# Kernel tuning notes

Measured on AMD Instinct MI355X. Metric: run time of the kernel, lower is better.

The kernel has to match this reference:

```python
import jax, jax.numpy as jnp
import numpy as np

EMBED_DIMS = [8, 16, 8]      # prod = 1024 = embed_dim
HIDDEN_DIMS = [16, 16, 16]   # prod = 4096 = hidden_dim
RANK = 16
B, S = 4, 1024


def _make_cores(key, in_dims, out_dims, rank):
    d = len(in_dims)
    ranks = [1] + [rank] * (d - 1) + [1]
    cores = []
    for k in range(d):
        key, sub = jax.random.split(key)
        shape = (ranks[k], in_dims[k], out_dims[k], ranks[k + 1])
        scale = 1.0 / np.sqrt(in_dims[k] * ranks[k])
        cores.append((scale * jax.random.normal(sub, shape, dtype=jnp.float32)))
    return cores


def setup_inputs() -> dict:
    key = jax.random.key(0)
    k_x, k1, k2, kb1, kb2 = jax.random.split(key, 5)
    x = jax.random.normal(k_x, (B, S, 1024), dtype=jnp.float32)
    fc1 = _make_cores(k1, EMBED_DIMS, HIDDEN_DIMS, RANK)
    fc2 = _make_cores(k2, HIDDEN_DIMS, EMBED_DIMS, RANK)
    b1 = 0.01 * jax.random.normal(kb1, (4096,), dtype=jnp.float32)
    b2 = 0.01 * jax.random.normal(kb2, (1024,), dtype=jnp.float32)
    return {
        "x": x,
        "fc1_c0": fc1[0], "fc1_c1": fc1[1], "fc1_c2": fc1[2], "fc1_b": b1,
        "fc2_c0": fc2[0], "fc2_c1": fc2[1], "fc2_c2": fc2[2], "fc2_b": b2,
    }


def tt_linear(x_flat, cores, bias, in_dims):
    """TT-matrix x batch-of-vectors product. x_flat: [N, prod(in_dims)].

    Cores: core_k has shape [r_{k-1}, n_k, m_k, r_k] with r_0 = r_d = 1.
    Invariant: acc is [r_{k-1}, n_k, rest] with rest laid out as
    (n_{k+1}..n_d, N, m_1..m_{k-1}).
    """
    N = x_flat.shape[0]
    acc = x_flat.reshape((N,) + tuple(in_dims))      # [N, n1..nd]
    acc = jnp.moveaxis(acc, 0, -1)                   # [n1..nd, N]
    acc = acc.reshape(in_dims[0], -1)[None]          # [1, n1, rest]
    d = len(cores)
    for k, c in enumerate(cores):
        # contract previous rank + current input mode
        acc = jnp.einsum('pnR,pnmq->Rmq', acc, c)    # [rest, m_k, r_k]
        if k < d - 1:
            n_next = in_dims[k + 1]
            R, m, q = acc.shape
            acc = acc.reshape(n_next, R // n_next, m, q)
            acc = jnp.transpose(acc, (3, 0, 1, 2)).reshape(q, n_next, -1)
    # final acc: [N * m1..m_{d-1}, m_d, 1] -> [N, M]
    return acc.reshape(N, -1) + bias


def reference(x, fc1_c0, fc1_c1, fc1_c2, fc1_b, fc2_c0, fc2_c1, fc2_c2, fc2_b):
    flat = x.reshape(-1, x.shape[-1])                        # [N, embed_dim]
    z1 = tt_linear(flat, [fc1_c0, fc1_c1, fc1_c2], fc1_b, EMBED_DIMS)   # [N, hidden]
    h1 = jax.nn.gelu(z1, approximate=False)                  # exact erf GELU (torch default)
    z2 = tt_linear(h1, [fc2_c0, fc2_c1, fc2_c2], fc2_b, HIDDEN_DIMS)    # [N, embed]
    return z2.reshape(*x.shape[:-1], z2.shape[-1])
```

## Files before the change

### kernel.cpp

```cpp
#include <hip/hip_runtime.h>
#include <stdint.h>

__device__ __forceinline__ float b2f(unsigned short u) {
    union { uint32_t i; float f; } v; v.i = ((uint32_t)u) << 16; return v.f;
}
__device__ __forceinline__ unsigned short f2b(float f) {
    union { float f; uint32_t i; } v; v.f = f;
    uint32_t r = v.i + 0x7fffu + ((v.i >> 16) & 1u);
    return (unsigned short)(r >> 16);
}

typedef __bf16 bf16x8 __attribute__((ext_vector_type(8)));
typedef float  f32x16 __attribute__((ext_vector_type(16)));

template<int N3, int M3>
__device__ __forceinline__ void build_T_body(int e,
                                             const float* __restrict__ c1,
                                             const float* __restrict__ c2,
                                             float* __restrict__ T) {
    int m3 = e % M3;
    int t  = e / M3;
    int n3 = t % N3;
    int rm = t / N3;
    float s = 0.f;
#pragma unroll
    for (int r2 = 0; r2 < 16; ++r2)
        s += c1[rm * 16 + r2] * c2[(r2 * N3 + n3) * M3 + m3];
    T[e] = s;
}

__global__ __launch_bounds__(256)
void prep_stage1(const float* __restrict__ c11, const float* __restrict__ c12,
                 float* __restrict__ T1,
                 const float* __restrict__ c21, const float* __restrict__ c22,
                 float* __restrict__ T2,
                 const float* __restrict__ x, unsigned short* __restrict__ xb) {
    const int b = blockIdx.x;
    if (b < 2048) {
        build_T_body<8, 16>(b * 256 + threadIdx.x, c11, c12, T1);
    } else if (b < 4096) {
        build_T_body<16, 8>((b - 2048) * 256 + threadIdx.x, c21, c22, T2);
    } else {
        const int t = (b - 4096) * 256 + threadIdx.x;
        const float4* p = (const float4*)(x + (size_t)t * 8);
        float4 f0 = p[0], f1 = p[1];
        int4 o;
        o.x = (uint32_t)f2b(f0.x) | ((uint32_t)f2b(f0.y) << 16);
        o.y = (uint32_t)f2b(f0.z) | ((uint32_t)f2b(f0.w) << 16);
        o.z = (uint32_t)f2b(f1.x) | ((uint32_t)f2b(f1.y) << 16);
        o.w = (uint32_t)f2b(f1.z) | ((uint32_t)f2b(f1.w) << 16);
        ((int4*)xb)[t] = o;
    }
}

template<int N1, int N2, int N3, int M1, int M2, int M3>
__device__ __forceinline__ void build_W_body(int t,
                                             const float* __restrict__ c0,
                                             const float* __restrict__ T,
                                             unsigned short* __restrict__ W) {
    constexpr int K = N1 * N2 * N3;
    int m3 = t % M3;
    int m2 = (t / M3) % M2;
    int n2 = (t / (M3 * M2)) % N2;
    int m1 = (t / (M3 * M2 * N2)) % M1;
    int n1 =  t / (M3 * M2 * N2 * M1);

    float c0r[16];
    const float4* c0p = (const float4*)(c0 + (n1 * M1 + m1) * 16);
#pragma unroll
    for (int i = 0; i < 4; ++i) ((float4*)c0r)[i] = c0p[i];

    float acc[N3] = {};
#pragma unroll
    for (int r1 = 0; r1 < 16; ++r1) {
        const float* Tp = T + (size_t)(((r1 * 16 + n2) * 16 + m2) * N3) * M3 + m3;
#pragma unroll
        for (int n3 = 0; n3 < N3; ++n3)
            acc[n3] += c0r[r1] * Tp[n3 * M3];
    }

    unsigned short ob[N3];
#pragma unroll
    for (int n3 = 0; n3 < N3; ++n3) ob[n3] = f2b(acc[n3]);

    unsigned short* dst = W + (size_t)((m1 * M2 + m2) * M3 + m3) * K
                            + (n1 * N2 + n2) * N3;
#pragma unroll
    for (int c = 0; c < N3 / 8; ++c)
        ((int4*)dst)[c] = ((const int4*)ob)[c];
}

__global__ __launch_bounds__(256)
void build_W_both(const float* __restrict__ c10, const float* __restrict__ T1,
                  unsigned short* __restrict__ W1,
                  const float* __restrict__ c20, const float* __restrict__ T2,
                  unsigned short* __restrict__ W2) {
    const int b = blockIdx.x;
    if (b < 2048)
        build_W_body<8, 16, 8, 16, 16, 16>(b * 256 + threadIdx.x, c10, T1, W1);
    else
        build_W_body<16, 16, 16, 8, 16, 8>((b - 2048) * 256 + threadIdx.x, c20, T2, W2);
}

template<int N1, int N2, int N3, int M1, int M2, int M3>
__global__ __launch_bounds__(256)
void build_W(const float* __restrict__ c0, const float* __restrict__ T,
             unsigned short* __restrict__ W) {
    build_W_body<N1, N2, N3, M1, M2, M3>(blockIdx.x * 256 + threadIdx.x, c0, T, W);
}

#define PC_COMPUTE(BUF)                                                       \
    {                                                                         \
        _Pragma("unroll")                                                     \
        for (int ks = 0; ks < 4; ++ks) {                                      \
            bf16x8 a_f[FI], b_f[FJ];                                          \
            _Pragma("unroll")                                                 \
            for (int i = 0; i < FI; ++i) {                                    \
                const int key = (m32 & 7) ^                                   \
                    (((waveM >> 3) + 4 * i + (m32 >> 3)) & 7);                \
                const int slot = ((ks * 2 + khalf) ^ key) * 8;                \
                a_f[i] = *(const bf16x8*)&As[(BUF) * ASZ +                    \
                          (waveM + i * 32 + m32) * BK + slot];                \
            }                                                                 \
            _Pragma("unroll")                                                 \
            for (int j = 0; j < FJ; ++j) {                                    \
                const int key = (m32 & 7) ^                                   \
                    (((waveN >> 3) + 4 * j + (m32 >> 3)) & 7);                \
                const int slot = ((ks * 2 + khalf) ^ key) * 8;                \
                b_f[j] = *(const bf16x8*)&Bs[(BUF) * BSZ +                    \
                          (waveN + j * 32 + m32) * BK + slot];                \
            }                                                                 \
            _Pragma("unroll")                                                 \
            for (int i = 0; i < FI; ++i)                                      \
                _Pragma("unroll")                                             \
                for (int j = 0; j < FJ; ++j)                                  \
                    acc[i][j] = __builtin_amdgcn_mfma_f32_32x32x16_bf16(      \
                        a_f[i], b_f[j], acc[i][j], 0, 0, 0);                  \
        }                                                                     \
    }

template<int BM, int BN, int KTOT, bool DO_GELU, bool A_F32, bool C_F32>
__global__ __launch_bounds__(512, 4)
void gemm_pc(const void* __restrict__ Av,
             const unsigned short* __restrict__ Bt,
             const float* __restrict__ bias,
             void* __restrict__ Cv,
             int Ncols) {
    constexpr int BK  = 64;
    constexpr int CA  = BM / 8;
    constexpr int CB  = BN / 8;
    constexpr int PA  = CA / 4;
    constexpr int PB  = CB / 4;
    constexpr int FI  = BM / 64;
    constexpr int FJ  = BN / 64;
    constexpr int ASZ = BM * BK;
    constexpr int BSZ = BN * BK;
    __shared__ unsigned short As[2 * ASZ];
    __shared__ unsigned short Bs[2 * BSZ];

    const int tid  = threadIdx.x;
    const int lane = tid & 63;
    const int wave = tid >> 6;
    const int rowBase = blockIdx.y * BM;
    const int colBase = blockIdx.x * BN;

    const int lr    = lane >> 3;
    const int jj    = lane & 7;
    const int m32   = lane & 31;
    const int khalf = lane >> 5;

    if (wave >= 4) {
        const int pw = wave - 4;

#pragma unroll
        for (int it = 0; it < PA; ++it) {
            const int c  = pw * PA + it;
            const int jg = jj ^ lr ^ (c & 7);
            const size_t aoff = (size_t)(rowBase + c * 8 + lr) * KTOT + jg * 8;
            int4 v;
            if (A_F32) {
                const float* ga = (const float*)Av + aoff;
                float4 f0 = *(const float4*)ga;
                float4 f1 = *(const float4*)(ga + 4);
                v.x = (uint32_t)f2b(f0.x) | ((uint32_t)f2b(f0.y) << 16);
                v.y = (uint32_t)f2b(f0.z) | ((uint32_t)f2b(f0.w) << 16);
                v.z = (uint32_t)f2b(f1.x) | ((uint32_t)f2b(f1.y) << 16);
                v.w = (uint32_t)f2b(f1.z) | ((uint32_t)f2b(f1.w) << 16);
            } else {
                v = *(const int4*)((const unsigned short*)Av + aoff);
            }
            *(int4*)&As[c * 512 + lane * 8] = v;
        }
#pragma unroll
        for (int it = 0; it < PB; ++it) {
            const int c  = pw * PB + it;
            const int jg = jj ^ lr ^ (c & 7);
            *(int4*)&Bs[c * 512 + lane * 8] =
                *(const int4*)(Bt + (size_t)(colBase + c * 8 + lr) * KTOT + jg * 8);
        }
        __syncthreads();

        int buf = 1;
        for (int k0 = BK; k0 < KTOT; k0 += BK) {
            int4 aR[PA], bR[PB];
#pragma unroll
            for (int it = 0; it < PA; ++it) {
                const int c  = pw * PA + it;
                const int jg = jj ^ lr ^ (c & 7);
                const size_t aoff = (size_t)(rowBase + c * 8 + lr) * KTOT + k0 + jg * 8;
                if (A_F32) {
                    const float* ga = (const float*)Av + aoff;
                    float4 f0 = *(const float4*)ga;
                    float4 f1 = *(const float4*)(ga + 4);
                    int4 v;
                    v.x = (uint32_t)f2b(f0.x) | ((uint32_t)f2b(f0.y) << 16);
                    v.y = (uint32_t)f2b(f0.z) | ((uint32_t)f2b(f0.w) << 16);
                    v.z = (uint32_t)f2b(f1.x) | ((uint32_t)f2b(f1.y) << 16);
                    v.w = (uint32_t)f2b(f1.z) | ((uint32_t)f2b(f1.w) << 16);
                    aR[it] = v;
                } else {
                    aR[it] = *(const int4*)((const unsigned short*)Av + aoff);
                }
            }
#pragma unroll
            for (int it = 0; it < PB; ++it) {
                const int c  = pw * PB + it;
                const int jg = jj ^ lr ^ (c & 7);
                bR[it] = *(const int4*)(Bt + (size_t)(colBase + c * 8 + lr) * KTOT + k0 + jg * 8);
            }
#pragma unroll
            for (int it = 0; it < PA; ++it) {
                const int c = pw * PA + it;
                *(int4*)&As[buf * ASZ + c * 512 + lane * 8] = aR[it];
            }
#pragma unroll
            for (int it = 0; it < PB; ++it) {
                const int c = pw * PB + it;
                *(int4*)&Bs[buf * BSZ + c * 512 + lane * 8] = bR[it];
            }
            __syncthreads();
            buf ^= 1;
        }
    } else {
        const int waveM = (wave >> 1) * (BM / 2);
        const int waveN = (wave & 1) * (BN / 2);
        f32x16 acc[FI][FJ] = {};

        __syncthreads();

        int cur = 0;
        for (int k0 = BK; k0 < KTOT; k0 += BK) {
            PC_COMPUTE(cur)
            __syncthreads();
            cur ^= 1;
        }
        PC_COMPUTE(cur)

#pragma unroll
        for (int i = 0; i < FI; ++i) {
#pragma unroll
            for (int j = 0; j < FJ; ++j) {
                const int col = colBase + waveN + j * 32 + m32;
                const float bv = bias[col];
#pragma unroll
                for (int reg = 0; reg < 16; ++reg) {
                    const int row = rowBase + waveM + i * 32 +
                                    (reg & 3) + 8 * (reg >> 2) + 4 * khalf;
                    float z = acc[i][j][reg] + bv;
                    if (DO_GELU)
                        z = 0.5f * z * (1.f + erff(z * 0.70710678118654752f));
                    const size_t off = (size_t)row * Ncols + col;
                    if (C_F32) ((float*)Cv)[off] = z;
                    else       ((unsigned short*)Cv)[off] = f2b(z);
                }
            }
        }
    }
}

extern "C" void kernel_launch(void* const* d_in, const int* in_sizes, int n_in,
                              void* d_out, int out_size, void* d_ws, size_t ws_size,
                              hipStream_t stream) {
    const float* x      = (const float*)d_in[0];
    const float* fc1_c0 = (const float*)d_in[1];
    const float* fc1_c1 = (const float*)d_in[2];
    const float* fc1_c2 = (const float*)d_in[3];
    const float* fc1_b  = (const float*)d_in[4];
    const float* fc2_c0 = (const float*)d_in[5];
    const float* fc2_c1 = (const float*)d_in[6];
    const float* fc2_c2 = (const float*)d_in[7];
    const float* fc2_b  = (const float*)d_in[8];

    float* T1 = (float*)d_out;
    float* T2 = (float*)d_out + 524288;
    unsigned short* xb = (unsigned short*)((char*)d_out + (4u << 20));

    char* ws = (char*)d_ws;
    const bool big = ws_size >= (48ull << 20);

    prep_stage1<<<6144, 256, 0, stream>>>(fc1_c1, fc1_c2, T1,
                                          fc2_c1, fc2_c2, T2, x, xb);

    if (big) {
        unsigned short* W1 = (unsigned short*)ws;
        unsigned short* W2 = (unsigned short*)(ws + (8u << 20));
        unsigned short* h  = (unsigned short*)(ws + (16u << 20));

        build_W_both<<<3072, 256, 0, stream>>>(fc1_c0, T1, W1,
                                               fc2_c0, T2, W2);
        gemm_pc<128, 128, 1024, true, false, false>
            <<<dim3(32, 32), 512, 0, stream>>>(xb, W1, fc1_b, h, 4096);
        gemm_pc<128, 64, 4096, false, false, true>
            <<<dim3(16, 32), 512, 0, stream>>>(h, W2, fc2_b, d_out, 1024);
    } else {
        unsigned short* W = (unsigned short*)ws;
        unsigned short* h = (unsigned short*)(ws + (8u << 20));

        build_W<8, 16, 8, 16, 16, 16><<<2048, 256, 0, stream>>>(fc1_c0, T1, W);
        gemm_pc<128, 128, 1024, true, false, false>
            <<<dim3(32, 32), 512, 0, stream>>>(xb, W, fc1_b, h, 4096);
        build_W<16, 16, 16, 8, 16, 8><<<1024, 256, 0, stream>>>(fc2_c0, T2, W);
        gemm_pc<128, 64, 4096, false, false, true>
            <<<dim3(16, 32), 512, 0, stream>>>(h, W, fc2_b, d_out, 1024);
    }
}
```

Measured before the change: 217.4 us.

## Replace producer-consumer GEMMs with direct global-to-LDS loads and block swizzle

Adds a new 256-thread GEMM kernel that stages A and B tiles with global_load_lds DMA into double-buffered dynamic shared memory, instead of using dedicated producer waves that copy through registers. It also remaps block indices so that neighbouring blocks are grouped for better L2 reuse, and it requests two blocks per CU. Both GEMMs on the large-workspace path now use this kernel. The trade-off is that every wave now handles both loading and MFMA work, and a single barrier per K-step may expose load latency.

```diff
diff --git a/kernel.cpp b/kernel.cpp
--- a/kernel.cpp
+++ b/kernel.cpp
@@ -107,6 +107,128 @@
 void build_W(const float* __restrict__ c0, const float* __restrict__ T,
              unsigned short* __restrict__ W) {
     build_W_body<N1, N2, N3, M1, M2, M3>(blockIdx.x * 256 + threadIdx.x, c0, T, W);
+}
+
+template<int BM, int BN, int KTOT, int GX, bool DO_GELU, bool C_F32>
+__global__ __launch_bounds__(256, 2)
+void gemm_gl(const unsigned short* __restrict__ A,
+             const unsigned short* __restrict__ Bt,
+             const float* __restrict__ bias,
+             void* __restrict__ Cv,
+             int Ncols)
+{
+    constexpr int BK   = 64;
+    constexpr int NT   = KTOT / BK;
+    constexpr int ASZ  = BM * BK;
+    constexpr int BSZ  = BN * BK;
+    constexpr int BUFE = ASZ + BSZ;
+    constexpr int ACH  = BM / 32;
+    constexpr int BCH  = BN / 32;
+    constexpr int FI   = BM / 64, FJ = BN / 64;
+
+    extern __shared__ unsigned short sh[];
+
+    const int tid   = threadIdx.x;
+    const int lane  = tid & 63;
+    const int wave  = tid >> 6;
+    const int m32   = lane & 31;
+    const int khalf = lane >> 5;
+    const int waveM = (wave >> 1) * (BM / 2);
+    const int waveN = (wave & 1) * (BN / 2);
+    const int srow  = tid >> 3;
+    const int sslot = tid & 7;
+
+    int lin = (int)blockIdx.y * GX + (int)blockIdx.x;
+    const int total = GX * (int)gridDim.y;
+    lin = (lin & 7) * (total >> 3) + (lin >> 3);
+    const int rowBase = (lin / GX) * BM;
+    const int colBase = (lin % GX) * BN;
+
+#define GL_STAGE(B_, K0_)                                                     \
+    {                                                                         \
+        _Pragma("unroll")                                                     \
+        for (int c = 0; c < ACH; ++c) {                                       \
+            const int r  = c * 32 + srow;                                     \
+            const int jg = sslot ^ (r & 7) ^ ((r >> 3) & 7);                  \
+            const unsigned short* src = A +                                   \
+                (size_t)(rowBase + r) * KTOT + (K0_) + jg * 8;                \
+            unsigned short* dst = sh + (B_) * BUFE + c * 2048 + wave * 512;   \
+            __builtin_amdgcn_global_load_lds(                                 \
+                (const __attribute__((address_space(1))) void*)src,           \
+                (__attribute__((address_space(3))) void*)dst, 16, 0, 0);      \
+        }                                                                     \
+        _Pragma("unroll")                                                     \
+        for (int c = 0; c < BCH; ++c) {                                       \
+            const int r  = c * 32 + srow;                                     \
+            const int jg = sslot ^ (r & 7) ^ ((r >> 3) & 7);                  \
+            const unsigned short* src = Bt +                                  \
+                (size_t)(colBase + r) * KTOT + (K0_) + jg * 8;                \
+            unsigned short* dst = sh + (B_) * BUFE + ASZ + c * 2048           \
+                                  + wave * 512;                               \
+            __builtin_amdgcn_global_load_lds(                                 \
+                (const __attribute__((address_space(1))) void*)src,           \
+                (__attribute__((address_space(3))) void*)dst, 16, 0, 0);      \
+        }                                                                     \
+    }
+
+    f32x16 acc[FI][FJ] = {};
+
+    GL_STAGE(0, 0)
+    __syncthreads();
+
+    int buf = 0;
+    for (int t = 0; t < NT; ++t) {
+        if (t + 1 < NT) GL_STAGE(buf ^ 1, (t + 1) * BK)
+
+        const unsigned short* Ab = sh + buf * BUFE;
+        const unsigned short* Bb = Ab + ASZ;
+#pragma unroll
+        for (int ks = 0; ks < 4; ++ks) {
+            bf16x8 a_f[FI], b_f[FJ];
+            const int g = ks * 2 + khalf;
+#pragma unroll
+            for (int i = 0; i < FI; ++i) {
+                const int r = waveM + i * 32 + m32;
+                const int key = (r & 7) ^ ((r >> 3) & 7);
+                a_f[i] = *(const bf16x8*)&Ab[r * BK + ((g ^ key) << 3)];
+            }
+#pragma unroll
+            for (int j = 0; j < FJ; ++j) {
+                const int r = waveN + j * 32 + m32;
+                const int key = (r & 7) ^ ((r >> 3) & 7);
+                b_f[j] = *(const bf16x8*)&Bb[r * BK + ((g ^ key) << 3)];
+            }
+#pragma unroll
+            for (int i = 0; i < FI; ++i)
+#pragma unroll
+                for (int j = 0; j < FJ; ++j)
+                    acc[i][j] = __builtin_amdgcn_mfma_f32_32x32x16_bf16(
+                        a_f[i], b_f[j], acc[i][j], 0, 0, 0);
+        }
+        __syncthreads();
+        buf ^= 1;
+    }
+#undef GL_STAGE
+
+#pragma unroll
+    for (int i = 0; i < FI; ++i) {
+#pragma unroll
+        for (int j = 0; j < FJ; ++j) {
+            const int col = colBase + waveN + j * 32 + m32;
+            const float bv = bias[col];
+#pragma unroll
+            for (int reg = 0; reg < 16; ++reg) {
+                const int row = rowBase + waveM + i * 32 +
+                                (reg & 3) + 8 * (reg >> 2) + 4 * khalf;
+                float z = acc[i][j][reg] + bv;
+                if (DO_GELU)
+                    z = 0.5f * z * (1.f + erff(z * 0.70710678118654752f));
+                const size_t off = (size_t)row * Ncols + col;
+                if (C_F32) ((float*)Cv)[off] = z;
+                else       ((unsigned short*)Cv)[off] = f2b(z);
+            }
+        }
+    }
 }
 
 #define PC_COMPUTE(BUF)                                                       \
@@ -171,7 +293,6 @@
 
     if (wave >= 4) {
         const int pw = wave - 4;
-
 #pragma unroll
         for (int it = 0; it < PA; ++it) {
             const int c  = pw * PA + it;
@@ -298,6 +419,21 @@
     char* ws = (char*)d_ws;
     const bool big = ws_size >= (48ull << 20);
 
+    constexpr int LDS1 = 2 * (128 + 128) * 64 * 2;
+    constexpr int LDS2 = 2 * (128 + 64) * 64 * 2;
+    static bool attr_done = false;
+    if (!attr_done) {
+        attr_done = true;
+        (void)hipFuncSetAttribute(
+            reinterpret_cast<const void*>(
+                &gemm_gl<128, 128, 1024, 32, true, false>),
+            hipFuncAttributeMaxDynamicSharedMemorySize, LDS1);
+        (void)hipFuncSetAttribute(
+            reinterpret_cast<const void*>(
+                &gemm_gl<128, 64, 4096, 16, false, true>),
+            hipFuncAttributeMaxDynamicSharedMemorySize, LDS2);
+    }
+
     prep_stage1<<<6144, 256, 0, stream>>>(fc1_c1, fc1_c2, T1,
                                           fc2_c1, fc2_c2, T2, x, xb);
 
@@ -308,10 +444,10 @@
 
         build_W_both<<<3072, 256, 0, stream>>>(fc1_c0, T1, W1,
                                                fc2_c0, T2, W2);
-        gemm_pc<128, 128, 1024, true, false, false>
-            <<<dim3(32, 32), 512, 0, stream>>>(xb, W1, fc1_b, h, 4096);
-        gemm_pc<128, 64, 4096, false, false, true>
-            <<<dim3(16, 32), 512, 0, stream>>>(h, W2, fc2_b, d_out, 1024);
+        gemm_gl<128, 128, 1024, 32, true, false>
+            <<<dim3(32, 32), 256, LDS1, stream>>>(xb, W1, fc1_b, h, 4096);
+        gemm_gl<128, 64, 4096, 16, false, true>
+            <<<dim3(16, 32), 256, LDS2, stream>>>(h, W2, fc2_b, d_out, 1024);
     } else {
         unsigned short* W = (unsigned short*)ws;
         unsigned short* h = (unsigned short*)(ws + (8u << 20));
```

After: 219.2 us. Within noise of the previous version (+0.8%).
